# Kernel optimization log

Measured on AMD Instinct MI355X. Metric: run time of the kernel, lower is better.

Reference implementation:

```python
import jax, jax.numpy as jnp
import numpy as np

B, S, D = 2, 2048, 4096
QH, KVH = 32, 8
HD = D // QH          # 128
KVD = KVH * HD        # 1024
GROUP = QH // KVH     # 4


def _make_freqs_cis(seq, hd):
    inv = 1.0 / (10000.0 ** (jnp.arange(0, hd, 2, dtype=jnp.float32) / hd))
    ang = jnp.outer(jnp.arange(seq, dtype=jnp.float32), inv)  # [S, HD//2]
    return jnp.stack([jnp.cos(ang), jnp.sin(ang)], axis=-1)    # [S, HD//2, 2]


def setup_inputs() -> dict:
    key = jax.random.key(0)
    ks = jax.random.split(key, 10)
    std = 0.02
    return {
        "xs": jax.random.normal(ks[0], (B, S, D), jnp.float32),
        "startpos": 0,
        "freqs_cis": _make_freqs_cis(S, HD),
        "Wq": jax.random.normal(ks[1], (D, D), jnp.float32) * std,
        "bq": jnp.zeros((D,), jnp.float32),
        "Wk": jax.random.normal(ks[2], (KVD, D), jnp.float32) * std,
        "bk": jnp.zeros((KVD,), jnp.float32),
        "Wv": jax.random.normal(ks[3], (KVD, D), jnp.float32) * std,
        "bv": jnp.zeros((KVD,), jnp.float32),
        "Wo": jax.random.normal(ks[4], (D, D), jnp.float32) * std,
        "bo": jnp.zeros((D,), jnp.float32),
    }


def _apply_rope(x, fc):
    # x: [B,S,H,HD], fc: [S, HD//2, 2] (cos,sin) -> complex multiply per pair
    xr = x.reshape(*x.shape[:-1], HD // 2, 2)
    cos = fc[None, :, None, :, 0]
    sin = fc[None, :, None, :, 1]
    out_r = xr[..., 0] * cos - xr[..., 1] * sin
    out_i = xr[..., 0] * sin + xr[..., 1] * cos
    return jnp.stack([out_r, out_i], axis=-1).reshape(x.shape)


def reference(xs, startpos, freqs_cis, Wq, bq, Wk, bk, Wv, bv, Wo, bo):
    b, s, _ = xs.shape
    q = (xs @ Wq.T + bq).reshape(b, s, QH, HD)
    k = (xs @ Wk.T + bk).reshape(b, s, KVH, HD)
    v = (xs @ Wv.T + bv).reshape(b, s, KVH, HD)

    fc = freqs_cis[startpos:startpos + s]
    q = _apply_rope(q, fc)
    k = _apply_rope(k, fc)
    # startpos == 0: cache write-then-read is identity on current k/v

    # GQA: group q heads per kv head; avoid materializing repeated K/V
    qg = q.transpose(0, 2, 1, 3).reshape(b, KVH, GROUP, s, HD)  # [b,kvh,g,s,d]
    kk = k.transpose(0, 2, 1, 3)                                 # [b,kvh,t,d]
    vv = v.transpose(0, 2, 1, 3)

    scale = 1.0 / jnp.sqrt(jnp.float32(HD))
    logits = jnp.einsum('bhgsd,bhtd->bhgst', qg, kk) * scale
    causal = jnp.tril(jnp.ones((s, s), dtype=bool))
    logits = jnp.where(causal[None, None, None], logits, jnp.float32(-1e30))
    probs = jax.nn.softmax(logits, axis=-1)
    ctx = jnp.einsum('bhgst,bhtd->bhgsd', probs, vv)             # [b,kvh,g,s,d]

    ctx = ctx.reshape(b, QH, s, HD).transpose(0, 2, 1, 3).reshape(b, s, D)
    return ctx @ Wo.T + bo
```

## Files before the change

### kernel.cpp

```cpp
#include <hip/hip_runtime.h>
#include <hip/hip_bf16.h>

typedef __bf16 bf16x8 __attribute__((ext_vector_type(8)));
typedef float  f32x4  __attribute__((ext_vector_type(4)));

#define MFMA(a, b, c) __builtin_amdgcn_mfma_f32_16x16x32_bf16((a), (b), (c), 0, 0, 0)

typedef __attribute__((address_space(1))) void* as1_vp;
typedef __attribute__((address_space(3))) void* as3_vp;

__device__ __forceinline__ void g2lds16(const void* g, void* lds) {
  __builtin_amdgcn_global_load_lds((as1_vp)(unsigned long long)g,
                                   (as3_vp)(unsigned int)(unsigned long long)lds,
                                   16, 0, 0);
}

__device__ __forceinline__ unsigned short bfbits(float x) {
  return __builtin_bit_cast(unsigned short, __float2bfloat16(x));
}

__global__ void cvt_f32_bf16(const float* __restrict__ in,
                             __hip_bfloat16* __restrict__ out, int n4) {
  int i = blockIdx.x * blockDim.x + threadIdx.x;
  if (i >= n4) return;
  float4 v = ((const float4*)in)[i];
  ushort4 u;
  u.x = bfbits(v.x); u.y = bfbits(v.y); u.z = bfbits(v.z); u.w = bfbits(v.w);
  ((ushort4*)out)[i] = u;
}

__global__ void concat_bias(const float* __restrict__ bq, const float* __restrict__ bk,
                            const float* __restrict__ bv, float* __restrict__ out) {
  int i = blockIdx.x * 256 + threadIdx.x;
  float v = (i < 4096) ? bq[i] : ((i < 5120) ? bk[i - 4096] : bv[i - 5120]);
  out[i] = v;
}

__global__ void rope_inplace(__hip_bfloat16* __restrict__ x, const float* __restrict__ fc,
                             const int* __restrict__ startpos, int pitch, int wshift,
                             long npairs) {
  long i = (long)blockIdx.x * blockDim.x + threadIdx.x;
  if (i >= npairs) return;
  int  wi    = (int)(i & ((1 << wshift) - 1));
  long token = i >> wshift;
  int  s  = (int)(token & 2047);
  int  j  = wi & 63;
  int  sp = startpos[0] + s;
  float c  = fc[(sp << 7) + (j << 1)];
  float sn = fc[(sp << 7) + (j << 1) + 1];
  long base = token * pitch + wi * 2;
  float xr = __bfloat162float(x[base]);
  float xi = __bfloat162float(x[base + 1]);
  x[base]     = __float2bfloat16(xr * c - xi * sn);
  x[base + 1] = __float2bfloat16(xr * sn + xi * c);
}

__global__ void transpose_v(const __hip_bfloat16* __restrict__ QKV,
                            __hip_bfloat16* __restrict__ VT) {
  __shared__ __hip_bfloat16 tile[32][33];
  int z = blockIdx.z, b = z >> 3, kvh = z & 7;
  int s0 = blockIdx.x * 32, h0 = blockIdx.y * 32;
  int tx = threadIdx.x, ty = threadIdx.y;
#pragma unroll
  for (int ry = ty; ry < 32; ry += 8)
    tile[ry][tx] =
        QKV[(long)(b * 2048 + s0 + ry) * 6144 + 5120 + kvh * 128 + h0 + tx];
  __syncthreads();
#pragma unroll
  for (int ry = ty; ry < 32; ry += 8)
    VT[((long)z * 128 + h0 + ry) * 2048 + s0 + tx] = tile[tx][ry];
}

#define BAR()  __builtin_amdgcn_s_barrier()
#define SB0()  __builtin_amdgcn_sched_barrier(0)
#define LGK0() do { asm volatile("s_waitcnt lgkmcnt(0)" ::: "memory"); \
                    __builtin_amdgcn_sched_barrier(0); } while (0)
#define VMC4() asm volatile("s_waitcnt vmcnt(4)" ::: "memory")
#define VMC0() asm volatile("s_waitcnt vmcnt(0)" ::: "memory")
#define PRI1() __builtin_amdgcn_s_setprio(1)
#define PRI0() __builtin_amdgcn_s_setprio(0)

template <int OUT_F32>
__global__ void __launch_bounds__(512, 2)
gemm256_bt(const __hip_bfloat16* __restrict__ A,
           const __hip_bfloat16* __restrict__ W,
           const float* __restrict__ bias,
           void* __restrict__ Cout, int M, int N, int K) {
  __shared__ __align__(16) char smem[131072];
  (void)M;
  const int t = threadIdx.x, w = t >> 6, l = t & 63, quad = l >> 4, lan = l & 15;
  const int wm = w >> 2, wn = w & 3;

  const int nwg = gridDim.x;
  const int xcd = blockIdx.x & 7, lid = blockIdx.x >> 3;
  const int qq = nwg >> 3, rr = nwg & 7;
  const int wg = (xcd < rr ? xcd * (qq + 1) : rr * (qq + 1) + (xcd - rr) * qq) + lid;
  const int ntn = N >> 8;
  const int bm = (wg / ntn) << 8, bn = (wg % ntn) << 8;

  const int csrc = ((t & 3) ^ ((t >> 3) & 3)) << 4;
  const char* aS0 = (const char*)(A + (long)(bm + (t >> 2)) * K) + csrc;
  const char* aS1 = aS0 + (long)K * 256;
  const char* bS0 = (const char*)(W + (long)(bn + (t >> 2)) * K) + csrc;
  const char* bS1 = bS0 + (long)K * 256;
  char* dA0 = smem + (w << 10);
  char* dA1 = smem + 16384 + (w << 10);
  char* dB0 = smem + 32768 + (w << 10);
  char* dB1 = smem + 49152 + (w << 10);

#define STG(src, dst, kt, bb)                                    \
  g2lds16((src) + (kt) * 128, (dst) + (bb) * 65536);             \
  g2lds16((src) + (kt) * 128 + 64, (dst) + (bb) * 65536 + 8192);

  const int rsw = (quad ^ ((lan >> 1) & 3)) << 4;
  const char* aR = smem + wm * 16384 + (lan << 6) + rsw;
  const char* bR = smem + 32768 + (wn >> 1) * 16384 + ((((wn & 1) << 6) + lan) << 6) + rsw;

  f32x4 acc[8][4] = {};
  bf16x8 fA[4][2], fB0[2][2], fB1[2][2];

#define RD_A(mb, bb)                                                          \
  _Pragma("unroll") for (int mm = 0; mm < 4; ++mm)                            \
  _Pragma("unroll") for (int j = 0; j < 2; ++j)                               \
    fA[mm][j] = *(const bf16x8*)(aR + (bb) * 65536 + ((mb) + mm) * 1024 + j * 8192);
#define RD_B(arr, nb, bb)                                                     \
  _Pragma("unroll") for (int nn = 0; nn < 2; ++nn)                            \
  _Pragma("unroll") for (int j = 0; j < 2; ++j)                               \
    arr[nn][j] = *(const bf16x8*)(bR + (bb) * 65536 + ((nb) + nn) * 1024 + j * 8192);
#define MM16(mb, arr, nb)                                                     \
  _Pragma("unroll") for (int mm = 0; mm < 4; ++mm)                            \
  _Pragma("unroll") for (int nn = 0; nn < 2; ++nn)                            \
  _Pragma("unroll") for (int j = 0; j < 2; ++j)                               \
    acc[(mb) + mm][(nb) + nn] = MFMA(fA[mm][j], arr[nn][j], acc[(mb) + mm][(nb) + nn]);

  STG(aS0, dA0, 0, 0); STG(aS1, dA1, 0, 0);
  STG(bS0, dB0, 0, 0); STG(bS1, dB1, 0, 0);
  STG(bS0, dB0, 1, 1); STG(bS1, dB1, 1, 1);
  VMC4();
  BAR();

  const int NT = K >> 6;
  for (int i = 0; i < (NT >> 1) - 1; ++i) {
    const int t0 = i << 1;
    RD_A(0, 0); RD_B(fB0, 0, 0);
    STG(aS0, dA0, t0 + 1, 1);
    SB0(); BAR(); LGK0();
    PRI1(); MM16(0, fB0, 0); PRI0();
    BAR();
    RD_B(fB1, 2, 0);
    STG(aS1, dA1, t0 + 1, 1);
    SB0(); BAR(); LGK0();
    PRI1(); MM16(0, fB1, 2); PRI0();
    BAR();
    RD_A(4, 0);
    STG(bS0, dB0, t0 + 2, 0);
    SB0(); BAR(); LGK0();
    PRI1(); MM16(4, fB0, 0); PRI0();
    BAR();
    STG(bS1, dB1, t0 + 2, 0);
    SB0(); BAR();
    PRI1(); MM16(4, fB1, 2); PRI0();
    VMC4();
    BAR();
    RD_A(0, 1); RD_B(fB0, 0, 1);
    STG(aS0, dA0, t0 + 2, 0);
    SB0(); BAR(); LGK0();
    PRI1(); MM16(0, fB0, 0); PRI0();
    BAR();
    RD_B(fB1, 2, 1);
    STG(aS1, dA1, t0 + 2, 0);
    SB0(); BAR(); LGK0();
    PRI1(); MM16(0, fB1, 2); PRI0();
    BAR();
    RD_A(4, 1);
    STG(bS0, dB0, t0 + 3, 1);
    SB0(); BAR(); LGK0();
    PRI1(); MM16(4, fB0, 0); PRI0();
    BAR();
    STG(bS1, dB1, t0 + 3, 1);
    SB0(); BAR();
    PRI1(); MM16(4, fB1, 2); PRI0();
    VMC4();
    BAR();
  }

  {
    RD_A(0, 0); RD_B(fB0, 0, 0);
    STG(aS0, dA0, NT - 1, 1);
    SB0(); BAR(); LGK0();
    PRI1(); MM16(0, fB0, 0); PRI0();
    BAR();
    RD_B(fB1, 2, 0);
    STG(aS1, dA1, NT - 1, 1);
    SB0(); BAR(); LGK0();
    PRI1(); MM16(0, fB1, 2); PRI0();
    BAR();
    RD_A(4, 0);
    SB0(); BAR(); LGK0();
    PRI1(); MM16(4, fB0, 0); PRI0();
    BAR();
    BAR();
    PRI1(); MM16(4, fB1, 2); PRI0();
    VMC0();
    BAR();
    RD_A(0, 1); RD_B(fB0, 0, 1);
    SB0(); BAR(); LGK0();
    PRI1(); MM16(0, fB0, 0); PRI0();
    BAR();
    RD_B(fB1, 2, 1);
    SB0(); BAR(); LGK0();
    PRI1(); MM16(0, fB1, 2); PRI0();
    BAR();
    RD_A(4, 1);
    SB0(); BAR(); LGK0();
    PRI1(); MM16(4, fB0, 0); PRI0();
    BAR();
    PRI1(); MM16(4, fB1, 2); PRI0();
  }

  float bsv[4];
#pragma unroll
  for (int n = 0; n < 4; ++n) bsv[n] = bias[bn + (wn << 6) + (n << 4) + lan];
#pragma unroll
  for (int m = 0; m < 8; ++m) {
#pragma unroll
    for (int e = 0; e < 4; ++e) {
      const long row = bm + (wm << 7) + (m << 4) + (quad << 2) + e;
#pragma unroll
      for (int n = 0; n < 4; ++n) {
        const float v = acc[m][n][e] + bsv[n];
        const long col = bn + (wn << 6) + (n << 4) + lan;
        if (OUT_F32) ((float*)Cout)[row * N + col] = v;
        else ((__hip_bfloat16*)Cout)[row * N + col] = __float2bfloat16(v);
      }
    }
  }
}
#undef STG
#undef RD_A
#undef RD_B
#undef MM16

__global__ void __launch_bounds__(256, 2) flash_attn(const __hip_bfloat16* __restrict__ QKV,
                                                     const __hip_bfloat16* __restrict__ VT,
                                                     __hip_bfloat16* __restrict__ Ctx, int S) {
  __shared__ __align__(16) char smem[50176];
  char* Ks = smem;
  char* Vs = smem + 16384;
  char* Ps = smem + 32768;
  const int t = threadIdx.x, w = t >> 6, l = t & 63, quad = l >> 4, lan = l & 15;
  const int b = blockIdx.z, qh = blockIdx.y, kvh = qh >> 2;
  const int q0idx = (int)gridDim.x - 1 - blockIdx.x;
  const int q0 = q0idx << 7;
  const float cl = 0.08838834764831845f * 1.4426950408889634f;

  {
    int rl = l >> 4, cd = l & 15;
#pragma unroll
    for (int ii = 0; ii < 8; ii++) {
      int i = (w << 3) + ii;
      int r = (i << 2) + rl;
      int cs = cd ^ (r & 15);
      const char* g =
          (const char*)(QKV + (long)(b * S + q0 + r) * 6144 + qh * 128) + (cs << 4);
      g2lds16(g, smem + (i << 10));
    }
  }
  __syncthreads();
  bf16x8 qf[2][4];
#pragma unroll
  for (int st = 0; st < 2; st++) {
    int row = ((((w << 1) + st) << 4) + lan);
#pragma unroll
    for (int ks = 0; ks < 4; ks++)
      qf[st][ks] = *(const bf16x8*)(smem + (row << 8) + ((((ks << 2) + quad) ^ lan) << 4));
  }

  f32x4 o[2][8] = {};
  float m0[2] = {-__builtin_inff(), -__builtin_inff()};
  float lsum[2] = {0.f, 0.f};
  const int ntiles = (q0idx << 1) + 2;

  for (int kt = 0; kt < ntiles; kt++) {
    const int t0 = kt << 6;
    __syncthreads();
    {
      int rl = l >> 4, cd = l & 15;
#pragma unroll
      for (int ii = 0; ii < 4; ii++) {
        int i = (w << 2) + ii;
        int r = (i << 2) + rl;
        int cs = cd ^ (r & 15);
        const char* g =
            (const char*)(QKV + (long)(b * S + t0 + r) * 6144 + 4096 + kvh * 128) + (cs << 4);
        g2lds16(g, Ks + (i << 10));
      }
      int dl = l >> 3, cd2 = l & 7;
#pragma unroll
      for (int ii = 0; ii < 4; ii++) {
        int i = (w << 2) + ii;
        int d = (i << 3) + dl;
        int cs = cd2 ^ dl;
        const char* g =
            (const char*)(VT + ((long)((b << 3) + kvh) * 128 + d) * S + t0) + (cs << 4);
        g2lds16(g, Vs + (i << 10));
      }
    }
    __syncthreads();

    f32x4 sa[2][4] = {{}, {}};
#pragma unroll
    for (int j = 0; j < 4; j++)
#pragma unroll
      for (int ks = 0; ks < 4; ks++) {
        bf16x8 kf = *(const bf16x8*)(Ks + (((j << 4) + lan) << 8) +
                                     ((((ks << 2) + quad) ^ lan) << 4));
        sa[0][j] = MFMA(kf, qf[0][ks], sa[0][j]);
        sa[1][j] = MFMA(kf, qf[1][ks], sa[1][j]);
      }

#pragma unroll
    for (int st = 0; st < 2; st++) {
      const int strip = (w << 1) + st;
      const int qg = q0 + (strip << 4) + lan;
      if (t0 + 63 > q0 + (strip << 4)) {
#pragma unroll
        for (int j = 0; j < 4; j++)
#pragma unroll
          for (int e = 0; e < 4; e++)
            if (t0 + (j << 4) + (quad << 2) + e > qg) sa[st][j][e] = -1e30f;
      }
      float mq = sa[st][0][0];
#pragma unroll
      for (int j = 0; j < 4; j++)
#pragma unroll
        for (int e = 0; e < 4; e++) mq = fmaxf(mq, sa[st][j][e]);
      mq = fmaxf(mq, __shfl_xor(mq, 16));
      mq = fmaxf(mq, __shfl_xor(mq, 32));
      float mn = fmaxf(m0[st], mq);
      float al = exp2f((m0[st] - mn) * cl);
      m0[st] = mn;
      float rs = 0.f;
      char* prow = Ps + strip * 2176 + lan * 136;
#pragma unroll
      for (int j = 0; j < 4; j++) {
        float p0 = exp2f((sa[st][j][0] - mn) * cl);
        float p1 = exp2f((sa[st][j][1] - mn) * cl);
        float p2 = exp2f((sa[st][j][2] - mn) * cl);
        float p3 = exp2f((sa[st][j][3] - mn) * cl);
        rs += (p0 + p1) + (p2 + p3);
        ushort4 u;
        u.x = bfbits(p0); u.y = bfbits(p1); u.z = bfbits(p2); u.w = bfbits(p3);
        *(ushort4*)(prow + (j << 5) + (quad << 3)) = u;
      }
      rs += __shfl_xor(rs, 16);
      rs += __shfl_xor(rs, 32);
      lsum[st] = lsum[st] * al + rs;
#pragma unroll
      for (int dt = 0; dt < 8; dt++) o[st][dt] *= al;
    }

    bf16x8 pf[2][2];
#pragma unroll
    for (int st = 0; st < 2; st++) {
      char* prow = Ps + ((w << 1) + st) * 2176 + lan * 136;
      pf[st][0] = *(const bf16x8*)(prow + (quad << 4));
      pf[st][1] = *(const bf16x8*)(prow + 64 + (quad << 4));
    }
#pragma unroll
    for (int dt = 0; dt < 8; dt++) {
      const int drow = (dt << 4) + lan;
#pragma unroll
      for (int ks = 0; ks < 2; ks++) {
        bf16x8 vf = *(const bf16x8*)(Vs + (drow << 7) +
                                     ((((ks << 2) + quad) ^ (lan & 7)) << 4));
        o[0][dt] = MFMA(vf, pf[0][ks], o[0][dt]);
        o[1][dt] = MFMA(vf, pf[1][ks], o[1][dt]);
      }
    }
  }

#pragma unroll
  for (int st = 0; st < 2; st++) {
    float inv = 1.0f / lsum[st];
    int strip = (w << 1) + st;
    long token = (long)b * S + q0 + (strip << 4) + lan;
    __hip_bfloat16* obase = Ctx + token * 4096 + qh * 128;
#pragma unroll
    for (int dt = 0; dt < 8; dt++) {
      ushort4 u;
      u.x = bfbits(o[st][dt][0] * inv);
      u.y = bfbits(o[st][dt][1] * inv);
      u.z = bfbits(o[st][dt][2] * inv);
      u.w = bfbits(o[st][dt][3] * inv);
      *(ushort4*)(obase + (dt << 4) + (quad << 2)) = u;
    }
  }
}

extern "C" void kernel_launch(void* const* d_in, const int* in_sizes, int n_in,
                              void* d_out, int out_size, void* d_ws, size_t ws_size,
                              hipStream_t stream) {
  const float* xs = (const float*)d_in[0];
  const int* startpos = (const int*)d_in[1];
  const float* fc = (const float*)d_in[2];
  const float* Wq = (const float*)d_in[3];
  const float* bq = (const float*)d_in[4];
  const float* Wk = (const float*)d_in[5];
  const float* bk = (const float*)d_in[6];
  const float* Wv = (const float*)d_in[7];
  const float* bv = (const float*)d_in[8];
  const float* Wo = (const float*)d_in[9];
  const float* bo = (const float*)d_in[10];
  float* out = (float*)d_out;
  char* ws = (char*)d_ws;

  __hip_bfloat16* Wqkvb = (__hip_bfloat16*)(ws);
  __hip_bfloat16* Xb    = (__hip_bfloat16*)(ws + 50331648L);
  __hip_bfloat16* QKVb  = (__hip_bfloat16*)(ws + 83886080L);
  __hip_bfloat16* VbT   = (__hip_bfloat16*)(ws + 134217728L);
  float*          bqkv  = (float*)(ws + 142606336L);
  __hip_bfloat16* Wob   = Wqkvb;
  __hip_bfloat16* Ctx   = Xb;

  cvt_f32_bf16<<<16384, 256, 0, stream>>>(xs, Xb, 4194304);
  cvt_f32_bf16<<<16384, 256, 0, stream>>>(Wq, Wqkvb, 4194304);
  cvt_f32_bf16<<<4096, 256, 0, stream>>>(Wk, Wqkvb + 16777216L, 1048576);
  cvt_f32_bf16<<<4096, 256, 0, stream>>>(Wv, Wqkvb + 20971520L, 1048576);
  concat_bias<<<24, 256, 0, stream>>>(bq, bk, bv, bqkv);

  gemm256_bt<0><<<dim3(384), 512, 0, stream>>>(Xb, Wqkvb, bqkv, QKVb, 4096, 6144, 4096);

  rope_inplace<<<32768, 256, 0, stream>>>(QKVb, fc, startpos, 6144, 11, 8388608L);
  rope_inplace<<<8192, 256, 0, stream>>>(QKVb + 4096, fc, startpos, 6144, 9, 2097152L);
  transpose_v<<<dim3(64, 4, 16), dim3(32, 8), 0, stream>>>(QKVb, VbT);
  cvt_f32_bf16<<<16384, 256, 0, stream>>>(Wo, Wob, 4194304);

  flash_attn<<<dim3(16, 32, 2), 256, 0, stream>>>(QKVb, VbT, Ctx, 2048);

  gemm256_bt<1><<<dim3(256), 512, 0, stream>>>(Ctx, Wob, bo, out, 4096, 4096, 4096);
}
```

Baseline: 825.4 us.

## Double-buffer K tiles and overlap V load with QK compute in flash attention

Splits K/V staging so the next K tile is prefetched into a second LDS buffer while the current one is used, and the V tile load overlaps the QK^T MFMAs and softmax, with fine-grained vmcnt waits in place of full syncthreads. MFMA sections are also wrapped in raised wave priority. The aim is to hide global-to-LDS latency behind compute. LDS per block grows from about 49KB to 65KB, which may reduce occupancy, and the relaxed barriers depend on correct vmcnt accounting.

Measured after the change: 808.9 us. 1.02x faster.

```diff
diff --git a/kernel.cpp b/kernel.cpp
--- a/kernel.cpp
+++ b/kernel.cpp
@@ -75,6 +75,7 @@
 #define SB0()  __builtin_amdgcn_sched_barrier(0)
 #define LGK0() do { asm volatile("s_waitcnt lgkmcnt(0)" ::: "memory"); \
                     __builtin_amdgcn_sched_barrier(0); } while (0)
+#define VMC8() asm volatile("s_waitcnt vmcnt(8)" ::: "memory")
 #define VMC4() asm volatile("s_waitcnt vmcnt(4)" ::: "memory")
 #define VMC0() asm volatile("s_waitcnt vmcnt(0)" ::: "memory")
 #define PRI1() __builtin_amdgcn_s_setprio(1)
@@ -244,10 +245,11 @@
 __global__ void __launch_bounds__(256, 2) flash_attn(const __hip_bfloat16* __restrict__ QKV,
                                                      const __hip_bfloat16* __restrict__ VT,
                                                      __hip_bfloat16* __restrict__ Ctx, int S) {
-  __shared__ __align__(16) char smem[50176];
-  char* Ks = smem;
-  char* Vs = smem + 16384;
-  char* Ps = smem + 32768;
+  __shared__ __align__(16) char smem[66560];
+  char* Ks0 = smem;
+  char* Ks1 = smem + 16384;
+  char* Vs  = smem + 32768;
+  char* Ps  = smem + 49152;
   const int t = threadIdx.x, w = t >> 6, l = t & 63, quad = l >> 4, lan = l & 15;
   const int b = blockIdx.z, qh = blockIdx.y, kvh = qh >> 2;
   const int q0idx = (int)gridDim.x - 1 - blockIdx.x;
@@ -275,49 +277,65 @@
     for (int ks = 0; ks < 4; ks++)
       qf[st][ks] = *(const bf16x8*)(smem + (row << 8) + ((((ks << 2) + quad) ^ lan) << 4));
   }
+  __syncthreads();
+
+  const int ntiles = (q0idx << 1) + 2;
+
+  auto stageK = [&](int kt, char* dst) {
+    int rl = l >> 4, cd = l & 15;
+#pragma unroll
+    for (int ii = 0; ii < 4; ii++) {
+      int i = (w << 2) + ii;
+      int r = (i << 2) + rl;
+      int cs = cd ^ (r & 15);
+      const char* g =
+          (const char*)(QKV + (long)(b * S + (kt << 6) + r) * 6144 + 4096 + kvh * 128) +
+          (cs << 4);
+      g2lds16(g, dst + (i << 10));
+    }
+  };
+  auto stageV = [&](int kt) {
+    int dl = l >> 3, cd2 = l & 7;
+#pragma unroll
+    for (int ii = 0; ii < 4; ii++) {
+      int i = (w << 2) + ii;
+      int d = (i << 3) + dl;
+      int cs = cd2 ^ dl;
+      const char* g =
+          (const char*)(VT + ((long)((b << 3) + kvh) * 128 + d) * S + (kt << 6)) + (cs << 4);
+      g2lds16(g, Vs + (i << 10));
+    }
+  };
 
   f32x4 o[2][8] = {};
   float m0[2] = {-__builtin_inff(), -__builtin_inff()};
   float lsum[2] = {0.f, 0.f};
-  const int ntiles = (q0idx << 1) + 2;
+
+  stageK(0, Ks0);
 
   for (int kt = 0; kt < ntiles; kt++) {
     const int t0 = kt << 6;
-    __syncthreads();
-    {
-      int rl = l >> 4, cd = l & 15;
-#pragma unroll
-      for (int ii = 0; ii < 4; ii++) {
-        int i = (w << 2) + ii;
-        int r = (i << 2) + rl;
-        int cs = cd ^ (r & 15);
-        const char* g =
-            (const char*)(QKV + (long)(b * S + t0 + r) * 6144 + 4096 + kvh * 128) + (cs << 4);
-        g2lds16(g, Ks + (i << 10));
-      }
-      int dl = l >> 3, cd2 = l & 7;
-#pragma unroll
-      for (int ii = 0; ii < 4; ii++) {
-        int i = (w << 2) + ii;
-        int d = (i << 3) + dl;
-        int cs = cd2 ^ dl;
-        const char* g =
-            (const char*)(VT + ((long)((b << 3) + kvh) * 128 + d) * S + t0) + (cs << 4);
-        g2lds16(g, Vs + (i << 10));
-      }
-    }
-    __syncthreads();
+    char* Kcur = (kt & 1) ? Ks1 : Ks0;
+    char* Knxt = (kt & 1) ? Ks0 : Ks1;
+    SB0(); BAR();
+    stageV(kt);
+    const int tn = (kt + 1 < ntiles) ? kt + 1 : kt;
+    stageK(tn, Knxt);
+    VMC8();
+    SB0(); BAR();
 
     f32x4 sa[2][4] = {{}, {}};
+    PRI1();
 #pragma unroll
     for (int j = 0; j < 4; j++)
 #pragma unroll
       for (int ks = 0; ks < 4; ks++) {
-        bf16x8 kf = *(const bf16x8*)(Ks + (((j << 4) + lan) << 8) +
+        bf16x8 kf = *(const bf16x8*)(Kcur + (((j << 4) + lan) << 8) +
                                      ((((ks << 2) + quad) ^ lan) << 4));
         sa[0][j] = MFMA(kf, qf[0][ks], sa[0][j]);
         sa[1][j] = MFMA(kf, qf[1][ks], sa[1][j]);
       }
+    PRI0();
 
 #pragma unroll
     for (int st = 0; st < 2; st++) {
@@ -367,6 +385,11 @@
       pf[st][0] = *(const bf16x8*)(prow + (quad << 4));
       pf[st][1] = *(const bf16x8*)(prow + 64 + (quad << 4));
     }
+
+    VMC4();
+    SB0(); BAR();
+
+    PRI1();
 #pragma unroll
     for (int dt = 0; dt < 8; dt++) {
       const int drow = (dt << 4) + lan;
@@ -378,6 +401,7 @@
         o[1][dt] = MFMA(vf, pf[1][ks], o[1][dt]);
       }
     }
+    PRI0();
   }
 
 #pragma unroll
```
